# Kernel optimization log

Hardware: AMD Instinct MI355X
Metric: run time of the kernel (lower is better)

The kernel has to match this reference:

```python
import jax, jax.numpy as jnp
import numpy as np


def setup_inputs() -> dict:
    key = jax.random.key(0)
    B, V = 2048, 32000
    input = jax.random.normal(key, (B, V), dtype=jnp.float32)
    return {"input": input}


def reference(input) -> jnp.ndarray:
    # Sparsemax along the last dim (self.dim == -1).
    x = input - jnp.max(input, axis=-1, keepdims=True)          # [B, V]
    zs = -jnp.sort(-x, axis=-1)                                  # descending sort [B, V]
    V = zs.shape[-1]
    range_values = jnp.arange(1, V + 1, dtype=x.dtype)           # [V]
    bound = 1.0 + range_values * zs                              # [B, V]
    cumsum_zs = jnp.cumsum(zs, axis=-1)                          # [B, V]
    is_gt = bound > cumsum_zs                                    # [B, V] bool
    k = jnp.sum(is_gt, axis=-1, keepdims=True).astype(x.dtype)   # [B, 1]
    k_idx = (k - 1.0).astype(jnp.int32)                          # [B, 1]
    taus = (jnp.take_along_axis(cumsum_zs, k_idx, axis=-1) - 1.0) / k  # [B, 1]
    return jnp.maximum(jnp.zeros_like(x), x - taus)
```

## Files before the change

kernel.cpp:

```cpp
#include <hip/hip_runtime.h>

#define THREADS 1024
#define NWAVES (THREADS / 64)
#define K4 8
#define CAP 2048

__global__ __launch_bounds__(THREADS, 2) void sparsemax_kernel(
    const float* __restrict__ in, float* __restrict__ out, int V)
{
    const int row = blockIdx.x;
    const float* __restrict__ x = in + (size_t)row * V;
    float* __restrict__ y = out + (size_t)row * V;
    const int tid  = threadIdx.x;
    const int lane = tid & 63;
    const int wave = tid >> 6;

    __shared__ float s_red[NWAVES];
    __shared__ float s_cand[CAP];
    __shared__ float s_sorted[CAP];
    __shared__ int   s_count;
    __shared__ float s_m;
    __shared__ float s_tau;
    __shared__ float s_sum;

    const int V4 = V >> 2;
    const float4* __restrict__ x4 = reinterpret_cast<const float4*>(x);
    float4* __restrict__ y4 = reinterpret_cast<float4*>(y);

    float4 d[K4];
    float lmax = -3.4e38f;
    #pragma unroll
    for (int k = 0; k < K4; ++k) {
        int i = k * THREADS + tid;
        if (i < V4) {
            float4 v = x4[i];
            d[k] = v;
            lmax = fmaxf(fmaxf(lmax, v.x), fmaxf(v.y, fmaxf(v.z, v.w)));
        } else {
            d[k] = make_float4(-3.4e38f, -3.4e38f, -3.4e38f, -3.4e38f);
        }
    }

    #pragma unroll
    for (int off = 32; off > 0; off >>= 1)
        lmax = fmaxf(lmax, __shfl_down(lmax, off, 64));
    if (lane == 0) s_red[wave] = lmax;
    __syncthreads();
    if (tid == 0) {
        float m = s_red[0];
        for (int w = 1; w < NWAVES; ++w) m = fmaxf(m, s_red[w]);
        s_m = m;
        s_count = 0;
    }
    __syncthreads();
    const float m = s_m;

    #pragma unroll
    for (int k = 0; k < K4; ++k) {
        float a[4] = {d[k].x, d[k].y, d[k].z, d[k].w};
        #pragma unroll
        for (int j = 0; j < 4; ++j) {
            float z = a[j] - m;
            if (z > -1.0f) {
                int p = atomicAdd(&s_count, 1);
                if (p < CAP) s_cand[p] = z;
            }
        }
    }
    __syncthreads();
    const int n = s_count;

    if (n <= CAP) {
        for (int i = tid; i < n; i += THREADS) {
            float zi = s_cand[i];
            int r = 0;
            for (int j = 0; j < n; ++j) {
                float zj = s_cand[j];
                r += (zj > zi) || (zj == zi && j < i);
            }
            s_sorted[r] = zi;
        }
        __syncthreads();
        if (tid == 0) {
            float cum = 0.0f;
            int k = 0;
            for (int j = 0; j < n; ++j) {
                cum += s_sorted[j];
                if (1.0f + (float)(j + 1) * s_sorted[j] > cum) k = j + 1;
            }
            float cumk = 0.0f;
            for (int j = 0; j < k; ++j) cumk += s_sorted[j];
            s_tau = (cumk - 1.0f) / (float)k;
        }
        __syncthreads();
    } else {
        float lo = -1.0f, hi = 0.0f;
        for (int it = 0; it < 48; ++it) {
            float mid = 0.5f * (lo + hi);
            float ls = 0.0f;
            #pragma unroll
            for (int k = 0; k < K4; ++k) {
                ls += fmaxf(0.0f, d[k].x - m - mid);
                ls += fmaxf(0.0f, d[k].y - m - mid);
                ls += fmaxf(0.0f, d[k].z - m - mid);
                ls += fmaxf(0.0f, d[k].w - m - mid);
            }
            #pragma unroll
            for (int off = 32; off > 0; off >>= 1)
                ls += __shfl_down(ls, off, 64);
            if (lane == 0) s_red[wave] = ls;
            __syncthreads();
            if (tid == 0) {
                float s = 0.0f;
                for (int w = 0; w < NWAVES; ++w) s += s_red[w];
                s_sum = s;
            }
            __syncthreads();
            float s = s_sum;
            __syncthreads();
            if (s > 1.0f) lo = mid; else hi = mid;
        }
        if (tid == 0) s_tau = 0.5f * (lo + hi);
        __syncthreads();
    }

    const float thr = s_m + s_tau;

    #pragma unroll
    for (int k = 0; k < K4; ++k) {
        int i = k * THREADS + tid;
        if (i < V4) {
            float4 o;
            o.x = fmaxf(0.0f, d[k].x - thr);
            o.y = fmaxf(0.0f, d[k].y - thr);
            o.z = fmaxf(0.0f, d[k].z - thr);
            o.w = fmaxf(0.0f, d[k].w - thr);
            y4[i] = o;
        }
    }
}

extern "C" void kernel_launch(void* const* d_in, const int* in_sizes, int n_in,
                              void* d_out, int out_size, void* d_ws, size_t ws_size,
                              hipStream_t stream) {
    const float* in = (const float*)d_in[0];
    float* out = (float*)d_out;
    const int V = 32000;
    const int B = in_sizes[0] / V;
    sparsemax_kernel<<<B, THREADS, 0, stream>>>(in, out, V);
}
```

Before: 446.7 us.

## Stream rows with running-max candidate filter, tiny sort, and sparse scatter output

Drops the 1024-thread register-resident row in favour of 256-thread blocks that stream the row in groups. Each wave keeps a running max and collects candidates above running-max minus one, storing both value and index. A second filter against the true max leaves a very small set (at most 128) to rank-sort. The output is written as a zero fill followed by a scatter of the few positive entries, which avoids keeping the row in registers and shrinks the O(n^2) sort. Rows with too many candidates fall back to a bisection that re-reads the input from global memory on every iteration, which would be expensive.

```diff
diff --git a/kernel.cpp b/kernel.cpp
--- a/kernel.cpp
+++ b/kernel.cpp
@@ -1,140 +1,160 @@
 #include <hip/hip_runtime.h>
 
-#define THREADS 1024
-#define NWAVES (THREADS / 64)
-#define K4 8
+#define THREADS 256
+#define NWAVES 4
 #define CAP 2048
+#define SMALLCAP 128
 
-__global__ __launch_bounds__(THREADS, 2) void sparsemax_kernel(
-    const float* __restrict__ in, float* __restrict__ out, int V)
+constexpr int kV  = 32000;
+constexpr int kV4 = kV / 4;
+
+__global__ __launch_bounds__(THREADS, 8) void sparsemax_kernel(
+    const float* __restrict__ in, float* __restrict__ out)
 {
     const int row = blockIdx.x;
-    const float* __restrict__ x = in + (size_t)row * V;
-    float* __restrict__ y = out + (size_t)row * V;
+    const float* __restrict__ x = in + (size_t)row * kV;
+    float* __restrict__ y = out + (size_t)row * kV;
     const int tid  = threadIdx.x;
     const int lane = tid & 63;
     const int wave = tid >> 6;
 
+    __shared__ float s_val[CAP];
+    __shared__ int   s_idx[CAP];
+    __shared__ float s_small[SMALLCAP];
+    __shared__ float s_sorted[SMALLCAP];
     __shared__ float s_red[NWAVES];
-    __shared__ float s_cand[CAP];
-    __shared__ float s_sorted[CAP];
-    __shared__ int   s_count;
+    __shared__ int   s_cnt;
+    __shared__ int   s_n2;
     __shared__ float s_m;
     __shared__ float s_tau;
     __shared__ float s_sum;
 
-    const int V4 = V >> 2;
+    if (tid == 0) { s_cnt = 0; s_n2 = 0; }
+    __syncthreads();
+
     const float4* __restrict__ x4 = reinterpret_cast<const float4*>(x);
-    float4* __restrict__ y4 = reinterpret_cast<float4*>(y);
 
-    float4 d[K4];
-    float lmax = -3.4e38f;
-    #pragma unroll
-    for (int k = 0; k < K4; ++k) {
-        int i = k * THREADS + tid;
-        if (i < V4) {
-            float4 v = x4[i];
-            d[k] = v;
-            lmax = fmaxf(fmaxf(lmax, v.x), fmaxf(v.y, fmaxf(v.z, v.w)));
-        } else {
-            d[k] = make_float4(-3.4e38f, -3.4e38f, -3.4e38f, -3.4e38f);
+    float wthr = -3.4e38f;
+    for (int g = 0; g < 8; ++g) {
+        float4 v[4];
+        float gmax = -3.4e38f;
+        #pragma unroll
+        for (int j = 0; j < 4; ++j) {
+            const int i = (g * 4 + j) * THREADS + tid;
+            if (i < kV4) {
+                v[j] = x4[i];
+                gmax = fmaxf(gmax, fmaxf(fmaxf(v[j].x, v[j].y), fmaxf(v[j].z, v[j].w)));
+            } else {
+                v[j] = make_float4(-3.4e38f, -3.4e38f, -3.4e38f, -3.4e38f);
+            }
+        }
+        #pragma unroll
+        for (int off = 32; off > 0; off >>= 1)
+            gmax = fmaxf(gmax, __shfl_xor(gmax, off, 64));
+        wthr = fmaxf(wthr, gmax);
+        const float cut = wthr - 1.0f;
+        #pragma unroll
+        for (int j = 0; j < 4; ++j) {
+            const int i = (g * 4 + j) * THREADS + tid;
+            if (i < kV4) {
+                const float a[4] = {v[j].x, v[j].y, v[j].z, v[j].w};
+                #pragma unroll
+                for (int c = 0; c < 4; ++c) {
+                    if (a[c] > cut) {
+                        int p = atomicAdd(&s_cnt, 1);
+                        if (p < CAP) { s_val[p] = a[c]; s_idx[p] = i * 4 + c; }
+                    }
+                }
+            }
         }
     }
 
-    #pragma unroll
-    for (int off = 32; off > 0; off >>= 1)
-        lmax = fmaxf(lmax, __shfl_down(lmax, off, 64));
-    if (lane == 0) s_red[wave] = lmax;
+    if (lane == 0) s_red[wave] = wthr;
     __syncthreads();
-    if (tid == 0) {
-        float m = s_red[0];
-        for (int w = 1; w < NWAVES; ++w) m = fmaxf(m, s_red[w]);
-        s_m = m;
-        s_count = 0;
-    }
+    if (tid == 0)
+        s_m = fmaxf(fmaxf(s_red[0], s_red[1]), fmaxf(s_red[2], s_red[3]));
     __syncthreads();
-    const float m = s_m;
+    const float m   = s_m;
+    const int   cnt = s_cnt;
 
-    #pragma unroll
-    for (int k = 0; k < K4; ++k) {
-        float a[4] = {d[k].x, d[k].y, d[k].z, d[k].w};
-        #pragma unroll
-        for (int j = 0; j < 4; ++j) {
-            float z = a[j] - m;
-            if (z > -1.0f) {
-                int p = atomicAdd(&s_count, 1);
-                if (p < CAP) s_cand[p] = z;
+    if (cnt <= CAP) {
+        const float cutf = m - 1.0f;
+        for (int c = tid; c < cnt; c += THREADS) {
+            const float vv = s_val[c];
+            if (vv > cutf) {
+                int p = atomicAdd(&s_n2, 1);
+                if (p < SMALLCAP) s_small[p] = vv - m;
             }
         }
+        __syncthreads();
+        const int n2 = s_n2;
+        if (n2 <= SMALLCAP) {
+            if (tid < n2) {
+                const float zi = s_small[tid];
+                int r = 0;
+                for (int j = 0; j < n2; ++j) {
+                    const float zj = s_small[j];
+                    r += (zj > zi) || (zj == zi && j < tid);
+                }
+                s_sorted[r] = zi;
+            }
+            __syncthreads();
+            if (tid == 0) {
+                float cum = 0.0f, cumk = 0.0f;
+                int k = 1;
+                for (int j = 0; j < n2; ++j) {
+                    cum += s_sorted[j];
+                    if (1.0f + (float)(j + 1) * s_sorted[j] > cum) { k = j + 1; cumk = cum; }
+                }
+                s_tau = (cumk - 1.0f) / (float)k;
+            }
+            __syncthreads();
+            const float thr = m + s_tau;
+
+            float4* __restrict__ y4 = reinterpret_cast<float4*>(y);
+            const float4 zero = make_float4(0.0f, 0.0f, 0.0f, 0.0f);
+            for (int i = tid; i < kV4; i += THREADS) y4[i] = zero;
+            __syncthreads();
+            for (int c = tid; c < cnt; c += THREADS) {
+                const float o = s_val[c] - thr;
+                if (o > 0.0f) y[s_idx[c]] = o;
+            }
+            return;
+        }
     }
-    __syncthreads();
-    const int n = s_count;
 
-    if (n <= CAP) {
-        for (int i = tid; i < n; i += THREADS) {
-            float zi = s_cand[i];
-            int r = 0;
-            for (int j = 0; j < n; ++j) {
-                float zj = s_cand[j];
-                r += (zj > zi) || (zj == zi && j < i);
-            }
-            s_sorted[r] = zi;
-        }
-        __syncthreads();
-        if (tid == 0) {
-            float cum = 0.0f;
-            int k = 0;
-            for (int j = 0; j < n; ++j) {
-                cum += s_sorted[j];
-                if (1.0f + (float)(j + 1) * s_sorted[j] > cum) k = j + 1;
-            }
-            float cumk = 0.0f;
-            for (int j = 0; j < k; ++j) cumk += s_sorted[j];
-            s_tau = (cumk - 1.0f) / (float)k;
-        }
-        __syncthreads();
-    } else {
+    {
         float lo = -1.0f, hi = 0.0f;
-        for (int it = 0; it < 48; ++it) {
-            float mid = 0.5f * (lo + hi);
+        for (int it = 0; it < 40; ++it) {
+            const float mid = 0.5f * (lo + hi);
             float ls = 0.0f;
-            #pragma unroll
-            for (int k = 0; k < K4; ++k) {
-                ls += fmaxf(0.0f, d[k].x - m - mid);
-                ls += fmaxf(0.0f, d[k].y - m - mid);
-                ls += fmaxf(0.0f, d[k].z - m - mid);
-                ls += fmaxf(0.0f, d[k].w - m - mid);
+            for (int i = tid; i < kV4; i += THREADS) {
+                const float4 vv = x4[i];
+                ls += fmaxf(0.0f, vv.x - m - mid);
+                ls += fmaxf(0.0f, vv.y - m - mid);
+                ls += fmaxf(0.0f, vv.z - m - mid);
+                ls += fmaxf(0.0f, vv.w - m - mid);
             }
             #pragma unroll
             for (int off = 32; off > 0; off >>= 1)
-                ls += __shfl_down(ls, off, 64);
+                ls += __shfl_xor(ls, off, 64);
             if (lane == 0) s_red[wave] = ls;
             __syncthreads();
-            if (tid == 0) {
-                float s = 0.0f;
-                for (int w = 0; w < NWAVES; ++w) s += s_red[w];
-                s_sum = s;
-            }
+            if (tid == 0) s_sum = s_red[0] + s_red[1] + s_red[2] + s_red[3];
             __syncthreads();
-            float s = s_sum;
+            const float s = s_sum;
             __syncthreads();
             if (s > 1.0f) lo = mid; else hi = mid;
         }
-        if (tid == 0) s_tau = 0.5f * (lo + hi);
-        __syncthreads();
-    }
-
-    const float thr = s_m + s_tau;
-
-    #pragma unroll
-    for (int k = 0; k < K4; ++k) {
-        int i = k * THREADS + tid;
-        if (i < V4) {
+        const float thr = m + 0.5f * (lo + hi);
+        float4* __restrict__ y4 = reinterpret_cast<float4*>(y);
+        for (int i = tid; i < kV4; i += THREADS) {
+            const float4 vv = x4[i];
             float4 o;
-            o.x = fmaxf(0.0f, d[k].x - thr);
-            o.y = fmaxf(0.0f, d[k].y - thr);
-            o.z = fmaxf(0.0f, d[k].z - thr);
-            o.w = fmaxf(0.0f, d[k].w - thr);
+            o.x = fmaxf(0.0f, vv.x - thr);
+            o.y = fmaxf(0.0f, vv.y - thr);
+            o.z = fmaxf(0.0f, vv.z - thr);
+            o.w = fmaxf(0.0f, vv.w - thr);
             y4[i] = o;
         }
     }
@@ -145,7 +165,6 @@
                               hipStream_t stream) {
     const float* in = (const float*)d_in[0];
     float* out = (float*)d_out;
-    const int V = 32000;
-    const int B = in_sizes[0] / V;
-    sparsemax_kernel<<<B, THREADS, 0, stream>>>(in, out, V);
+    const int B = in_sizes[0] / kV;
+    sparsemax_kernel<<<B, THREADS, 0, stream>>>(in, out);
 }
```

Result: slower. 639.8 us (+43.2%).
